# Kernel optimization log

Hardware: AMD Instinct MI355X
Metric: run time of the kernel (lower is better)

Reference implementation:

```python
import jax, jax.numpy as jnp
import numpy as np


def _pairwise_dist(a, b):
    # a: [B, N, D], b: [B, M, D] -> Euclidean distances [B, N, M]
    aa = jnp.sum(a * a, axis=-1)  # [B, N]
    bb = jnp.sum(b * b, axis=-1)  # [B, M]
    ab = jnp.einsum('bnd,bmd->bnm', a, b)  # [B, N, M]
    d2 = aa[:, :, None] + bb[None if aa.ndim == 1 else slice(None), None, :].reshape(bb.shape[0], 1, bb.shape[1]) - 2.0 * ab
    return jnp.sqrt(jnp.maximum(d2, 0.0))


def setup_inputs() -> dict:
    key = jax.random.key(0)
    k1, k2 = jax.random.split(key)
    B, N, M, D = 4, 8192, 8192, 3
    inp = jax.random.normal(k1, (B, N, D), dtype=jnp.float32)
    tgt = jax.random.normal(k2, (B, M, D), dtype=jnp.float32)
    return {"input": inp, "target": tgt}


def reference(input, target):
    # Bidirectional Chamfer distance, matching the torch module:
    # for each batch element (inner call has batch_size=1):
    #   distances1 = NN dist of each target point to input cloud (tree1=input, query array2=target)
    #   distances2 = NN dist of each input point to target cloud
    #   per-sample loss = mean(distances1) + mean(distances2)
    # total loss = sum over batch.
    d = _pairwise_dist(input, target)  # [B, N, M]
    nn_for_target = jnp.min(d, axis=1)  # [B, M] closest input point per target point
    nn_for_input = jnp.min(d, axis=2)   # [B, N] closest target point per input point
    per_sample = jnp.mean(nn_for_target, axis=1) + jnp.mean(nn_for_input, axis=1)  # [B]
    return jnp.sum(per_sample)
```

## Files before the change

### kernel.cpp

```cpp
#include <hip/hip_runtime.h>
#include <math.h>


typedef __attribute__((ext_vector_type(8)))  _Float16 f16x8;
typedef __attribute__((ext_vector_type(16))) float    f32x16;

constexpr int TPB    = 256;
constexpr int NPTS   = 8192;
constexpr int NB     = 4;
constexpr int MSPLIT = 8;
constexpr int SLICE  = NPTS / MSPLIT;
constexpr int TILES  = SLICE / 32;
constexpr int QPB    = 256;

__device__ inline float max3f(float a, float b, float c) {
    return fmaxf(fmaxf(a, b), c);
}

__device__ inline float merge16(float run, f32x16 v) {
    const float w0 = max3f(v[0],  v[1],  v[2]);
    const float w1 = max3f(v[3],  v[4],  v[5]);
    const float w2 = max3f(v[6],  v[7],  v[8]);
    const float w3 = max3f(v[9],  v[10], v[11]);
    const float w4 = max3f(v[12], v[13], v[14]);
    const float x0 = max3f(w0, w1, v[15]);
    const float x1 = max3f(w2, w3, w4);
    return max3f(run, x0, x1);
}

__device__ inline f16x8 make_qfrag(float x, float y, float z, int half) {
    const _Float16 hx = (_Float16)x, hy = (_Float16)y, hz = (_Float16)z;
    const _Float16 lx = (_Float16)(x - (float)hx);
    const _Float16 ly = (_Float16)(y - (float)hy);
    const _Float16 lz = (_Float16)(z - (float)hz);
    const f16x8 f0 = (f16x8){hx, hy, hz, hx, hy, hz, lx, ly};
    const f16x8 f1 = (f16x8){lz, (_Float16)1.0f, (_Float16)1.0f, 0, 0, 0, 0, 0};
    return half ? f1 : f0;
}

__global__ __launch_bounds__(TPB) void prep_frags(
    const float* __restrict__ inp, const float* __restrict__ tgt,
    f16x8* __restrict__ frag, float* __restrict__ out)
{
    const int idx = blockIdx.x * TPB + threadIdx.x;
    if (idx == 0) *out = 0.0f;
    const int rl    = idx & 31;
    const int half  = (idx >> 5) & 1;
    const int tile  = (idx >> 6) & 255;
    const int cb    = idx >> 14;
    const int cloud = cb >> 2;
    const int b     = cb & 3;
    const int r     = tile * 32 + rl;
    const float* src = (cloud ? tgt : inp) + ((size_t)b * NPTS + r) * 3;
    const float x = src[0], y = src[1], z = src[2];
    const _Float16 hx = (_Float16)x, hy = (_Float16)y, hz = (_Float16)z;
    const _Float16 lx = (_Float16)(x - (float)hx);
    const _Float16 ly = (_Float16)(y - (float)hy);
    const _Float16 lz = (_Float16)(z - (float)hz);
    const float c = 0.5f * (x * x + y * y + z * z);
    const _Float16 chi = (_Float16)c;
    const _Float16 clo = (_Float16)(c - (float)chi);
    const _Float16 nchi = -chi, nclo = -clo;
    f16x8 f;
    if (half == 0) f = (f16x8){hx, hy, hz, lx, ly, lz, hx, hy};
    else           f = (f16x8){hz, nchi, nclo, 0, 0, 0, 0, 0};
    frag[idx] = f;
}

__global__ __launch_bounds__(TPB) void chamfer_nn_mfma(
    const float* __restrict__ inp, const float* __restrict__ tgt,
    const f16x8* __restrict__ frag, float* __restrict__ partial)
{
    const int z    = blockIdx.z;
    const int dir  = z >> 2;
    const int b    = z & 3;
    const int s    = blockIdx.y;
    const int tid  = threadIdx.x;
    const int w    = tid >> 6;
    const int lane = tid & 63;
    const int half = lane >> 5;
    const int col  = lane & 31;

    __shared__ f16x8 lds[2048];

    {
        const int refcloud = dir ? 0 : 1;
        const f16x8* g = frag + ((size_t)(refcloud * 4 + b) * 16384
                                 + (size_t)s * (TILES * 64));
#pragma unroll
        for (int i = 0; i < 8; ++i) {
            __builtin_amdgcn_global_load_lds(
                (const void*)(g + i * 256 + w * 64 + lane),
                (void*)&lds[i * 256 + w * 64],
                16, 0, 0);
        }
    }

    const float* qb = (dir ? tgt : inp) + (size_t)b * NPTS * 3;
    const int qbase = blockIdx.x * QPB + w * 64;
    const int q0 = qbase + col, q1 = q0 + 32;
    const float x0 = qb[q0 * 3 + 0], y0 = qb[q0 * 3 + 1], z0 = qb[q0 * 3 + 2];
    const float x1 = qb[q1 * 3 + 0], y1 = qb[q1 * 3 + 1], z1 = qb[q1 * 3 + 2];
    const float cq0 = 0.5f * (x0 * x0 + y0 * y0 + z0 * z0);
    const float cq1 = 0.5f * (x1 * x1 + y1 * y1 + z1 * z1);
    const f16x8 bq0 = make_qfrag(x0, y0, z0, half);
    const f16x8 bq1 = make_qfrag(x1, y1, z1, half);

    __syncthreads();

    const f32x16 zf = (f32x16)0.0f;
    float run0 = -3.4e38f, run1 = -3.4e38f;
#pragma unroll 4
    for (int t = 0; t < TILES; ++t) {
        const f16x8 a = lds[t * 64 + lane];
        const f32x16 acc0 = __builtin_amdgcn_mfma_f32_32x32x16_f16(a, bq0, zf, 0, 0, 0);
        const f32x16 acc1 = __builtin_amdgcn_mfma_f32_32x32x16_f16(a, bq1, zf, 0, 0, 0);
        run0 = merge16(run0, acc0);
        run1 = merge16(run1, acc1);
    }

    run0 = fmaxf(run0, __shfl_xor(run0, 32));
    run1 = fmaxf(run1, __shfl_xor(run1, 32));

    if (lane < 32) {
        float* p = partial + ((size_t)z * MSPLIT + s) * NPTS;
        p[q0] = cq0 - run0;
        p[q1] = cq1 - run1;
    }
}

__global__ __launch_bounds__(256) void reduce_mfma(
    const float* __restrict__ partial, float* __restrict__ out, float inv)
{
    const int i = blockIdx.x * 256 + threadIdx.x;
    const float* p = partial + ((size_t)(i >> 13) * MSPLIT) * NPTS + (i & (NPTS - 1));
    float v = p[0];
#pragma unroll
    for (int sl = 1; sl < MSPLIT; ++sl) v = fminf(v, p[(size_t)sl * NPTS]);
    float sacc = sqrtf(fmaxf(2.0f * v, 0.0f)) * inv;
#pragma unroll
    for (int off = 32; off > 0; off >>= 1) sacc += __shfl_down(sacc, off, 64);
    __shared__ float wsum[4];
    const int lane = threadIdx.x & 63, wid = threadIdx.x >> 6;
    if (lane == 0) wsum[wid] = sacc;
    __syncthreads();
    if (threadIdx.x == 0) atomicAdd(out, wsum[0] + wsum[1] + wsum[2] + wsum[3]);
}

__global__ __launch_bounds__(TPB) void chamfer_nn_valu(
    const float* __restrict__ A, const float* __restrict__ Bp,
    unsigned int* __restrict__ minA, unsigned int* __restrict__ minB,
    int N, int M, int B)
{
    const int bz = blockIdx.z, b = bz % B, dir = bz / B;
    const float* Q = dir ? Bp : A;
    const float* R = dir ? A : Bp;
    unsigned int* om = dir ? minB : minA;
    const int NQ = dir ? M : N, NR = dir ? N : M;
    const int mSlice = NR / gridDim.y;
    const int tid = threadIdx.x;
    const int nBase = blockIdx.x * (TPB * 4);
    const int mStart = blockIdx.y * mSlice;
    const float* qb = Q + (size_t)b * NQ * 3;
    const float* rb = R + (size_t)b * NR * 3;
    float qx[4], qy[4], qz[4], dmax[4];
#pragma unroll
    for (int k = 0; k < 4; ++k) {
        const int n = nBase + tid + k * TPB;
        qx[k] = qb[n * 3]; qy[k] = qb[n * 3 + 1]; qz[k] = qb[n * 3 + 2];
        dmax[k] = -3.4e38f;
    }
    __shared__ float4 tgtl[256];
    for (int m0 = mStart; m0 < mStart + mSlice; m0 += 256) {
        __syncthreads();
        {
            const float* src = rb + (size_t)(m0 + tid) * 3;
            const float rx = src[0], ry = src[1], rz = src[2];
            tgtl[tid] = make_float4(rx, ry, rz,
                -0.5f * fmaf(rz, rz, fmaf(ry, ry, rx * rx)));
        }
        __syncthreads();
#pragma unroll 2
        for (int j = 0; j < 256; j += 2) {
            const float4 r0 = tgtl[j], r1 = tgtl[j + 1];
#pragma unroll
            for (int k = 0; k < 4; ++k) {
                const float t0 = fmaf(qz[k], r0.z, fmaf(qy[k], r0.y, fmaf(qx[k], r0.x, r0.w)));
                const float t1 = fmaf(qz[k], r1.z, fmaf(qy[k], r1.y, fmaf(qx[k], r1.x, r1.w)));
                dmax[k] = max3f(dmax[k], t0, t1);
            }
        }
    }
#pragma unroll
    for (int k = 0; k < 4; ++k) {
        const int n = nBase + tid + k * TPB;
        const float c = 0.5f * fmaf(qz[k], qz[k], fmaf(qy[k], qy[k], qx[k] * qx[k]));
        atomicMin(&om[(size_t)b * NQ + n], __float_as_uint(fmaxf(c - dmax[k], 0.0f)));
    }
}

__global__ __launch_bounds__(256) void chamfer_reduce(
    const unsigned int* __restrict__ mins, int nA, int nTotal,
    float scaleA, float scaleB, float* __restrict__ out)
{
    float s = 0.0f;
    for (int i = blockIdx.x * blockDim.x + threadIdx.x; i < nTotal;
         i += gridDim.x * blockDim.x) {
        s += sqrtf(2.0f * __uint_as_float(mins[i])) * (i < nA ? scaleA : scaleB);
    }
#pragma unroll
    for (int off = 32; off > 0; off >>= 1) s += __shfl_down(s, off, 64);
    __shared__ float wsum[4];
    const int lane = threadIdx.x & 63, wid = threadIdx.x >> 6;
    if (lane == 0) wsum[wid] = s;
    __syncthreads();
    if (threadIdx.x == 0) atomicAdd(out, wsum[0] + wsum[1] + wsum[2] + wsum[3]);
}

extern "C" void kernel_launch(void* const* d_in, const int* in_sizes, int n_in,
                              void* d_out, int out_size, void* d_ws, size_t ws_size,
                              hipStream_t stream) {
    const float* inp = (const float*)d_in[0];
    const float* tgt = (const float*)d_in[1];
    float* out = (float*)d_out;

    const int B = 4, D = 3;
    const int N = in_sizes[0] / (B * D);
    const int M = in_sizes[1] / (B * D);

    const size_t fragBytes    = (size_t)131072 * 16;
    const size_t partialBytes = (size_t)8 * MSPLIT * NPTS * 4;

    if (N == NPTS && M == NPTS && B == NB &&
        ws_size >= fragBytes + partialBytes) {
        f16x8* frag    = (f16x8*)d_ws;
        float* partial = (float*)((char*)d_ws + fragBytes);
        prep_frags<<<dim3(131072 / TPB), TPB, 0, stream>>>(inp, tgt, frag, out);
        dim3 grid(NPTS / QPB, MSPLIT, 8);
        chamfer_nn_mfma<<<grid, TPB, 0, stream>>>(inp, tgt, frag, partial);
        reduce_mfma<<<dim3(65536 / 256), 256, 0, stream>>>(
            partial, out, 1.0f / NPTS);
    } else {
        unsigned int* min_in  = (unsigned int*)d_ws;
        unsigned int* min_tgt = min_in + (size_t)B * N;
        hipMemsetAsync(d_ws, 0xFF,
                       (size_t)(B * N + B * M) * sizeof(unsigned int), stream);
        hipMemsetAsync(d_out, 0, sizeof(float), stream);
        dim3 grid(N / (TPB * 4), 32, 2 * B);
        chamfer_nn_valu<<<grid, TPB, 0, stream>>>(inp, tgt, min_in, min_tgt, N, M, B);
        chamfer_reduce<<<dim3(64), 256, 0, stream>>>(
            min_in, B * N, B * (N + M), 1.0f / N, 1.0f / M, out);
    }
}
```

Before: 88.16 us.

## Fuse fragment prep, NN search and reduction into one double-buffered MFMA kernel

Replaces the three-kernel pipeline (global fragment prep, M-split MFMA NN search writing partials, min/sum reduce) with a single kernel. Each block now scans the full reference cloud in 1024-point chunks, converting points to f16 hi/lo fragments in LDS with a double buffer, and reduces sqrt distances directly into an atomic. This removes the workspace round trips and two launches. In exchange each block does a long serial loop with only one query column per wave and a grid of 256 blocks of 512 threads, so parallelism and MFMA reuse per A-fragment load are lower.

```diff
diff --git a/kernel.cpp b/kernel.cpp
--- a/kernel.cpp
+++ b/kernel.cpp
@@ -5,13 +5,13 @@
 typedef __attribute__((ext_vector_type(8)))  _Float16 f16x8;
 typedef __attribute__((ext_vector_type(16))) float    f32x16;
 
-constexpr int TPB    = 256;
+constexpr int TPB    = 512;
 constexpr int NPTS   = 8192;
 constexpr int NB     = 4;
-constexpr int MSPLIT = 8;
-constexpr int SLICE  = NPTS / MSPLIT;
-constexpr int TILES  = SLICE / 32;
 constexpr int QPB    = 256;
+constexpr int CHUNK  = 1024;
+constexpr int NCHUNK = NPTS / CHUNK;
+constexpr int TILES  = CHUNK / 32;
 
 __device__ inline float max3f(float a, float b, float c) {
     return fmaxf(fmaxf(a, b), c);
@@ -38,116 +38,98 @@
     return half ? f1 : f0;
 }
 
-__global__ __launch_bounds__(TPB) void prep_frags(
-    const float* __restrict__ inp, const float* __restrict__ tgt,
-    f16x8* __restrict__ frag, float* __restrict__ out)
-{
-    const int idx = blockIdx.x * TPB + threadIdx.x;
-    if (idx == 0) *out = 0.0f;
-    const int rl    = idx & 31;
-    const int half  = (idx >> 5) & 1;
-    const int tile  = (idx >> 6) & 255;
-    const int cb    = idx >> 14;
-    const int cloud = cb >> 2;
-    const int b     = cb & 3;
-    const int r     = tile * 32 + rl;
-    const float* src = (cloud ? tgt : inp) + ((size_t)b * NPTS + r) * 3;
-    const float x = src[0], y = src[1], z = src[2];
+__device__ inline void write_ref(f16x8* buf, int r, float x, float y, float z) {
     const _Float16 hx = (_Float16)x, hy = (_Float16)y, hz = (_Float16)z;
     const _Float16 lx = (_Float16)(x - (float)hx);
     const _Float16 ly = (_Float16)(y - (float)hy);
     const _Float16 lz = (_Float16)(z - (float)hz);
-    const float c = 0.5f * (x * x + y * y + z * z);
+    const float c = 0.5f * fmaf(z, z, fmaf(y, y, x * x));
     const _Float16 chi = (_Float16)c;
     const _Float16 clo = (_Float16)(c - (float)chi);
-    const _Float16 nchi = -chi, nclo = -clo;
-    f16x8 f;
-    if (half == 0) f = (f16x8){hx, hy, hz, lx, ly, lz, hx, hy};
-    else           f = (f16x8){hz, nchi, nclo, 0, 0, 0, 0, 0};
-    frag[idx] = f;
-}
-
-__global__ __launch_bounds__(TPB) void chamfer_nn_mfma(
+    const int base = (r >> 5) * 64 + (r & 31);
+    buf[base]      = (f16x8){hx, hy, hz, lx, ly, lz, hx, hy};
+    buf[base + 32] = (f16x8){hz, -chi, -clo, 0, 0, 0, 0, 0};
+}
+
+__global__ __launch_bounds__(TPB) void chamfer_one(
     const float* __restrict__ inp, const float* __restrict__ tgt,
-    const f16x8* __restrict__ frag, float* __restrict__ partial)
+    float* __restrict__ out)
 {
-    const int z    = blockIdx.z;
-    const int dir  = z >> 2;
-    const int b    = z & 3;
-    const int s    = blockIdx.y;
+    const int dir = blockIdx.y >> 2;
+    const int b   = blockIdx.y & 3;
+    const float* qb = (dir ? tgt : inp) + (size_t)b * NPTS * 3;
+    const float* rb = (dir ? inp : tgt) + (size_t)b * NPTS * 3;
+
     const int tid  = threadIdx.x;
     const int w    = tid >> 6;
     const int lane = tid & 63;
     const int half = lane >> 5;
     const int col  = lane & 31;
 
-    __shared__ f16x8 lds[2048];
+    const int q = blockIdx.x * QPB + w * 32 + col;
+    const float qx = qb[q * 3 + 0], qy = qb[q * 3 + 1], qz = qb[q * 3 + 2];
+    const f16x8 bq = make_qfrag(qx, qy, qz, half);
+
+    __shared__ f16x8 lds[2 * 2048];
 
     {
-        const int refcloud = dir ? 0 : 1;
-        const f16x8* g = frag + ((size_t)(refcloud * 4 + b) * 16384
-                                 + (size_t)s * (TILES * 64));
-#pragma unroll
-        for (int i = 0; i < 8; ++i) {
-            __builtin_amdgcn_global_load_lds(
-                (const void*)(g + i * 256 + w * 64 + lane),
-                (void*)&lds[i * 256 + w * 64],
-                16, 0, 0);
-        }
-    }
-
-    const float* qb = (dir ? tgt : inp) + (size_t)b * NPTS * 3;
-    const int qbase = blockIdx.x * QPB + w * 64;
-    const int q0 = qbase + col, q1 = q0 + 32;
-    const float x0 = qb[q0 * 3 + 0], y0 = qb[q0 * 3 + 1], z0 = qb[q0 * 3 + 2];
-    const float x1 = qb[q1 * 3 + 0], y1 = qb[q1 * 3 + 1], z1 = qb[q1 * 3 + 2];
-    const float cq0 = 0.5f * (x0 * x0 + y0 * y0 + z0 * z0);
-    const float cq1 = 0.5f * (x1 * x1 + y1 * y1 + z1 * z1);
-    const f16x8 bq0 = make_qfrag(x0, y0, z0, half);
-    const f16x8 bq1 = make_qfrag(x1, y1, z1, half);
-
+        const float* s0 = rb + (size_t)tid * 3;
+        const float* s1 = rb + (size_t)(512 + tid) * 3;
+        write_ref(lds, tid,       s0[0], s0[1], s0[2]);
+        write_ref(lds, 512 + tid, s1[0], s1[1], s1[2]);
+    }
     __syncthreads();
 
     const f32x16 zf = (f32x16)0.0f;
-    float run0 = -3.4e38f, run1 = -3.4e38f;
+    float run = -3.4e38f;
+
+    for (int c = 0; c < NCHUNK; ++c) {
+        f16x8* bufR = lds + (c & 1) * 2048;
+        f16x8* bufW = lds + ((c & 1) ^ 1) * 2048;
+
+        float nx0 = 0, ny0 = 0, nz0 = 0, nx1 = 0, ny1 = 0, nz1 = 0;
+        const bool more = (c + 1 < NCHUNK);
+        if (more) {
+            const float* s0 = rb + (size_t)((c + 1) * CHUNK + tid) * 3;
+            const float* s1 = rb + (size_t)((c + 1) * CHUNK + 512 + tid) * 3;
+            nx0 = s0[0]; ny0 = s0[1]; nz0 = s0[2];
+            nx1 = s1[0]; ny1 = s1[1]; nz1 = s1[2];
+        }
+
 #pragma unroll 4
-    for (int t = 0; t < TILES; ++t) {
-        const f16x8 a = lds[t * 64 + lane];
-        const f32x16 acc0 = __builtin_amdgcn_mfma_f32_32x32x16_f16(a, bq0, zf, 0, 0, 0);
-        const f32x16 acc1 = __builtin_amdgcn_mfma_f32_32x32x16_f16(a, bq1, zf, 0, 0, 0);
-        run0 = merge16(run0, acc0);
-        run1 = merge16(run1, acc1);
-    }
-
-    run0 = fmaxf(run0, __shfl_xor(run0, 32));
-    run1 = fmaxf(run1, __shfl_xor(run1, 32));
-
-    if (lane < 32) {
-        float* p = partial + ((size_t)z * MSPLIT + s) * NPTS;
-        p[q0] = cq0 - run0;
-        p[q1] = cq1 - run1;
-    }
-}
-
-__global__ __launch_bounds__(256) void reduce_mfma(
-    const float* __restrict__ partial, float* __restrict__ out, float inv)
-{
-    const int i = blockIdx.x * 256 + threadIdx.x;
-    const float* p = partial + ((size_t)(i >> 13) * MSPLIT) * NPTS + (i & (NPTS - 1));
-    float v = p[0];
-#pragma unroll
-    for (int sl = 1; sl < MSPLIT; ++sl) v = fminf(v, p[(size_t)sl * NPTS]);
-    float sacc = sqrtf(fmaxf(2.0f * v, 0.0f)) * inv;
-#pragma unroll
-    for (int off = 32; off > 0; off >>= 1) sacc += __shfl_down(sacc, off, 64);
-    __shared__ float wsum[4];
-    const int lane = threadIdx.x & 63, wid = threadIdx.x >> 6;
-    if (lane == 0) wsum[wid] = sacc;
+        for (int t = 0; t < TILES; ++t) {
+            const f16x8 a = bufR[t * 64 + lane];
+            const f32x16 acc =
+                __builtin_amdgcn_mfma_f32_32x32x16_f16(a, bq, zf, 0, 0, 0);
+            run = merge16(run, acc);
+        }
+
+        if (more) {
+            write_ref(bufW, tid,       nx0, ny0, nz0);
+            write_ref(bufW, 512 + tid, nx1, ny1, nz1);
+        }
+        __syncthreads();
+    }
+
+    run = fmaxf(run, __shfl_xor(run, 32));
+    const float cq = 0.5f * fmaf(qz, qz, fmaf(qy, qy, qx * qx));
+    const float sval = fmaxf(cq - run, 0.0f);
+    float term = (lane < 32) ? sqrtf(2.0f * sval) * (1.0f / NPTS) : 0.0f;
+#pragma unroll
+    for (int off = 32; off > 0; off >>= 1) term += __shfl_down(term, off, 64);
+
+    float* bs = (float*)lds;
+    if (lane == 0) bs[w] = term;
     __syncthreads();
-    if (threadIdx.x == 0) atomicAdd(out, wsum[0] + wsum[1] + wsum[2] + wsum[3]);
-}
-
-__global__ __launch_bounds__(TPB) void chamfer_nn_valu(
+    if (tid == 0) {
+        float s = 0.0f;
+#pragma unroll
+        for (int i = 0; i < 8; ++i) s += bs[i];
+        atomicAdd(out, s);
+    }
+}
+
+__global__ __launch_bounds__(256) void chamfer_nn_valu(
     const float* __restrict__ A, const float* __restrict__ Bp,
     unsigned int* __restrict__ minA, unsigned int* __restrict__ minB,
     int N, int M, int B)
@@ -159,14 +141,14 @@
     const int NQ = dir ? M : N, NR = dir ? N : M;
     const int mSlice = NR / gridDim.y;
     const int tid = threadIdx.x;
-    const int nBase = blockIdx.x * (TPB * 4);
+    const int nBase = blockIdx.x * (256 * 4);
     const int mStart = blockIdx.y * mSlice;
     const float* qb = Q + (size_t)b * NQ * 3;
     const float* rb = R + (size_t)b * NR * 3;
     float qx[4], qy[4], qz[4], dmax[4];
 #pragma unroll
     for (int k = 0; k < 4; ++k) {
-        const int n = nBase + tid + k * TPB;
+        const int n = nBase + tid + k * 256;
         qx[k] = qb[n * 3]; qy[k] = qb[n * 3 + 1]; qz[k] = qb[n * 3 + 2];
         dmax[k] = -3.4e38f;
     }
@@ -193,7 +175,7 @@
     }
 #pragma unroll
     for (int k = 0; k < 4; ++k) {
-        const int n = nBase + tid + k * TPB;
+        const int n = nBase + tid + k * 256;
         const float c = 0.5f * fmaf(qz[k], qz[k], fmaf(qy[k], qy[k], qx[k] * qx[k]));
         atomicMin(&om[(size_t)b * NQ + n], __float_as_uint(fmaxf(c - dmax[k], 0.0f)));
     }
@@ -228,26 +210,18 @@
     const int N = in_sizes[0] / (B * D);
     const int M = in_sizes[1] / (B * D);
 
-    const size_t fragBytes    = (size_t)131072 * 16;
-    const size_t partialBytes = (size_t)8 * MSPLIT * NPTS * 4;
-
-    if (N == NPTS && M == NPTS && B == NB &&
-        ws_size >= fragBytes + partialBytes) {
-        f16x8* frag    = (f16x8*)d_ws;
-        float* partial = (float*)((char*)d_ws + fragBytes);
-        prep_frags<<<dim3(131072 / TPB), TPB, 0, stream>>>(inp, tgt, frag, out);
-        dim3 grid(NPTS / QPB, MSPLIT, 8);
-        chamfer_nn_mfma<<<grid, TPB, 0, stream>>>(inp, tgt, frag, partial);
-        reduce_mfma<<<dim3(65536 / 256), 256, 0, stream>>>(
-            partial, out, 1.0f / NPTS);
+    if (N == NPTS && M == NPTS && B == NB) {
+        hipMemsetAsync(d_out, 0, sizeof(float), stream);
+        dim3 grid(NPTS / QPB, 2 * NB);
+        chamfer_one<<<grid, TPB, 0, stream>>>(inp, tgt, out);
     } else {
         unsigned int* min_in  = (unsigned int*)d_ws;
         unsigned int* min_tgt = min_in + (size_t)B * N;
         hipMemsetAsync(d_ws, 0xFF,
                        (size_t)(B * N + B * M) * sizeof(unsigned int), stream);
         hipMemsetAsync(d_out, 0, sizeof(float), stream);
-        dim3 grid(N / (TPB * 4), 32, 2 * B);
-        chamfer_nn_valu<<<grid, TPB, 0, stream>>>(inp, tgt, min_in, min_tgt, N, M, B);
+        dim3 grid(N / (256 * 4), 32, 2 * B);
+        chamfer_nn_valu<<<grid, 256, 0, stream>>>(inp, tgt, min_in, min_tgt, N, M, B);
         chamfer_reduce<<<dim3(64), 256, 0, stream>>>(
             min_in, B * N, B * (N + M), 1.0f / N, 1.0f / M, out);
     }
```

New measurement: 75.88 us. 1.16x faster.
